# Kernel tuning notes

Hardware: AMD Instinct MI355X
Metric: run time of the kernel (lower is better)

## Reference

```python
import jax, jax.numpy as jnp
import numpy as np

B, N, E, A, H, F, HEADS = 2, 16384, 262144, 3, 128, 16, 4
DH = H // HEADS
CONST = (2.0 * np.pi) ** 0.5


def setup_inputs() -> dict:
    key = jax.random.key(0)
    ks = jax.random.split(key, 16)
    s = 0.05
    return {
        "x": jax.random.normal(ks[0], (B, N, H), jnp.float32),
        "edge_index": jax.random.randint(ks[1], (2, E), 0, N),
        # per-action message MLPs (self.mlp)
        "mlp_W1": jax.random.normal(ks[2], (A, H, H), jnp.float32) * s,
        "mlp_b1": jnp.zeros((A, H), jnp.float32),
        "mlp_W2": jax.random.normal(ks[3], (A, H, H), jnp.float32) * s,
        "mlp_b2": jnp.zeros((A, H), jnp.float32),
        # transformer (MMTs) projections, 4 heads over the action axis
        "Wq": jax.random.normal(ks[4], (H, H), jnp.float32) * s,
        "bq": jnp.zeros((H,), jnp.float32),
        "Wk": jax.random.normal(ks[5], (H, H), jnp.float32) * s,
        "bk": jnp.zeros((H,), jnp.float32),
        "Wv": jax.random.normal(ks[6], (H, H), jnp.float32) * s,
        "bv": jnp.zeros((H,), jnp.float32),
        "Wo": jax.random.normal(ks[7], (H, H), jnp.float32) * s,
        "bo": jnp.zeros((H,), jnp.float32),
        # decide_mu MLPs (decide_In_sigma is never used in the original forward)
        "mu_W1": jax.random.normal(ks[8], (A, H, H), jnp.float32) * s,
        "mu_b1": jnp.zeros((A, H), jnp.float32),
        "mu_W2": jax.random.normal(ks[9], (A, H, F), jnp.float32) * s,
        "mu_b2": jnp.zeros((A, F), jnp.float32),
    }


def _forward(x, edge_index, mlp_W1, mlp_b1, mlp_W2, mlp_b2,
             Wq, bq, Wk, bk, Wv, bv, Wo, bo, mu_W1, mu_b1, mu_W2, mu_b2):
    # per-action MLP stack: (B,N,H) -> (B,N,A,H)
    h = jax.nn.relu(jnp.einsum('bnh,ahk->bnak', x, mlp_W1) + mlp_b1)
    h = jnp.einsum('bnak,akh->bnah', h, mlp_W2) + mlp_b2
    # gather along source nodes, scatter-add into destination bins
    dst, src = edge_index[0], edge_index[1]
    g = h[:, src]                                   # (B,E,A,H) ~ 800 MB
    agg = jax.ops.segment_sum(jnp.moveaxis(g, 1, 0), dst, num_segments=N)
    agg = jnp.moveaxis(agg, 0, 1)                   # (B,N,A,H)
    # multi-head self-attention over the action axis (len A) per node
    q = (jnp.einsum('bnah,hk->bnak', agg, Wq) + bq).reshape(B, N, A, HEADS, DH)
    k = (jnp.einsum('bnah,hk->bnak', agg, Wk) + bk).reshape(B, N, A, HEADS, DH)
    v = (jnp.einsum('bnah,hk->bnak', agg, Wv) + bv).reshape(B, N, A, HEADS, DH)
    scores = jnp.einsum('bnqed,bnked->bneqk', q, k) / (DH ** 0.5)
    attn = jax.nn.softmax(scores, axis=-1)
    o = jnp.einsum('bneqk,bnked->bnqed', attn, v).reshape(B, N, A, H)
    h_I = agg + jnp.einsum('bnah,hk->bnak', o, Wo) + bo  # residual
    # per-action decode to action means: (B,N,A,F)
    m = jax.nn.relu(jnp.einsum('bnah,ahk->bnak', h_I, mu_W1) + mu_b1)
    mu = jnp.einsum('bnak,akf->bnaf', m, mu_W2) + mu_b2
    # Gaussian reparameterized sampling, VAR is a non-trainable all-ones buffer
    VAR = jnp.ones((N, A, F), jnp.float32)
    noise = jax.random.normal(jax.random.key(42), mu.shape, mu.dtype)
    sample = mu + noise * VAR
    logp = -jnp.log(CONST * VAR) - (sample - mu) ** 2 / (2.0 * VAR ** 2)
    a0 = jax.nn.softmax(jnp.tanh(sample[:, :, 0, :]), axis=-1)
    a1 = jax.nn.sigmoid(sample[:, :, 1, :])
    a2 = jnp.tanh(sample[:, :, 2, :])
    sample_out = jnp.stack([a0, a1, a2], axis=2)    # (B,N,A,F)
    return sample_out, logp.sum((-1, -2))           # ((B,N,A,F),(B,N))


def reference(x, edge_index, mlp_W1, mlp_b1, mlp_W2, mlp_b2,
              Wq, bq, Wk, bk, Wv, bv, Wo, bo, mu_W1, mu_b1, mu_W2, mu_b2):
    return _forward(x, edge_index, mlp_W1, mlp_b1, mlp_W2, mlp_b2,
                    Wq, bq, Wk, bk, Wv, bv, Wo, bo, mu_W1, mu_b1, mu_W2, mu_b2)
```

## Files before the change

kernel.cpp:

```cpp
#include <hip/hip_runtime.h>

#define NN    16384
#define EE    262144
#define BNODES 32768
#define AH    384
#define TOT_NOISE 1572864u

typedef __attribute__((ext_vector_type(8))) short short8;
typedef __attribute__((ext_vector_type(4))) float v4f;

__device__ __forceinline__ unsigned short f2bf(float f) {
  unsigned u = __float_as_uint(f);
  unsigned r = u + 0x7fffu + ((u >> 16) & 1u);
  return (unsigned short)(r >> 16);
}
__device__ __forceinline__ float bf2f(unsigned short h) {
  return __uint_as_float(((unsigned)h) << 16);
}
__device__ __forceinline__ float bflo(unsigned u) { return __uint_as_float(u << 16); }
__device__ __forceinline__ float bfhi(unsigned u) { return __uint_as_float(u & 0xffff0000u); }

__device__ __forceinline__ void threefry2x32_042(unsigned& x0, unsigned& x1) {
  const unsigned ks0 = 0u;
  const unsigned ks1 = 42u;
  const unsigned ks2 = 0x1BD11BDAu ^ 0u ^ 42u;
  x0 += ks0; x1 += ks1;
#define TFR(r) { x0 += x1; x1 = (x1 << (r)) | (x1 >> (32 - (r))); x1 ^= x0; }
  TFR(13) TFR(15) TFR(26) TFR(6)   x0 += ks1; x1 += ks2 + 1u;
  TFR(17) TFR(29) TFR(16) TFR(24)  x0 += ks2; x1 += ks0 + 2u;
  TFR(13) TFR(15) TFR(26) TFR(6)   x0 += ks0; x1 += ks1 + 3u;
  TFR(17) TFR(29) TFR(16) TFR(24)  x0 += ks1; x1 += ks2 + 4u;
  TFR(13) TFR(15) TFR(26) TFR(6)   x0 += ks2; x1 += ks0 + 5u;
#undef TFR
}

__device__ __forceinline__ float erfinv_f32(float x) {
  float w = -log1pf(-x * x);
  float p;
  if (w < 5.0f) {
    w -= 2.5f;
    p = 2.81022636e-08f;
    p = fmaf(p, w, 3.43273939e-07f);
    p = fmaf(p, w, -3.5233877e-06f);
    p = fmaf(p, w, -4.39150654e-06f);
    p = fmaf(p, w, 0.00021858087f);
    p = fmaf(p, w, -0.00125372503f);
    p = fmaf(p, w, -0.00417768164f);
    p = fmaf(p, w, 0.246640727f);
    p = fmaf(p, w, 1.50140941f);
  } else {
    w = sqrtf(w) - 3.0f;
    p = -0.000200214257f;
    p = fmaf(p, w, 0.000100950558f);
    p = fmaf(p, w, 0.00134934322f);
    p = fmaf(p, w, -0.00367342844f);
    p = fmaf(p, w, 0.00573950773f);
    p = fmaf(p, w, -0.0076224613f);
    p = fmaf(p, w, 0.00943887047f);
    p = fmaf(p, w, 1.00167406f);
    p = fmaf(p, w, 2.83297682f);
  }
  return p * x;
}

__device__ __forceinline__ unsigned jax_random_bits32(unsigned i) {
  unsigned x0 = 0u, x1 = i;
  threefry2x32_042(x0, x1);
  return x0 ^ x1;
}

__device__ __forceinline__ float jax_normal_from_bits(unsigned bits) {
  float f = __uint_as_float((bits >> 9) | 0x3f800000u) - 1.0f;
  const float lo = -0.99999994f;
  float u = f * 2.0f + lo;
  u = fmaxf(u, lo);
  return 1.4142135623730951f * erfinv_f32(u);
}

__global__ void edge_count(const int* __restrict__ dst, int* __restrict__ deg) {
  int e = blockIdx.x * 256 + threadIdx.x;
  if (e < EE) atomicAdd(&deg[dst[e]], 1);
}

__global__ __launch_bounds__(256) void scan_k(const int* __restrict__ deg,
                                              int* __restrict__ offs,
                                              int* __restrict__ cur) {
  __shared__ int part[256];
  int t = threadIdx.x;
  int base = t * 64;
  int s = 0;
  for (int i = 0; i < 64; i++) s += deg[base + i];
  part[t] = s;
  __syncthreads();
  for (int off = 1; off < 256; off <<= 1) {
    int v = (t >= off) ? part[t - off] : 0;
    __syncthreads();
    part[t] += v;
    __syncthreads();
  }
  int run = (t == 0) ? 0 : part[t - 1];
  for (int i = 0; i < 64; i++) {
    offs[base + i] = run;
    cur[base + i] = run;
    run += deg[base + i];
  }
  if (t == 255) offs[NN] = run;
}

__global__ void edge_fill(const int* __restrict__ dst, const int* __restrict__ srcv,
                          int* __restrict__ cur, int* __restrict__ csr) {
  int e = blockIdx.x * 256 + threadIdx.x;
  if (e < EE) {
    int d = dst[e];
    int p = atomicAdd(&cur[d], 1);
    csr[p] = srcv[e];
  }
}

__global__ __launch_bounds__(256) void prep_wfrag(
    const float* __restrict__ W1, const float* __restrict__ W2,
    const float* __restrict__ mW1,
    const float* __restrict__ Wq, const float* __restrict__ Wk,
    const float* __restrict__ Wv, const float* __restrict__ Wo,
    unsigned short* __restrict__ F) {
  int m = blockIdx.y;
  const float* W;
  if (m < 3) W = W1 + (long)m * 16384;
  else if (m < 6) W = W2 + (long)(m - 3) * 16384;
  else if (m < 9) W = mW1 + (long)(m - 6) * 16384;
  else W = (m == 9) ? Wq : (m == 10) ? Wk : (m == 11) ? Wv : Wo;
  int f = blockIdx.x * 256 + threadIdx.x;
  int tile = f >> 9;
  int kt = tile >> 3, nt = tile & 7;
  int r = f & 511;
  int lane = r >> 3, j = r & 7;
  int k = kt * 32 + (lane >> 4) * 8 + j;
  int n = nt * 16 + (lane & 15);
  F[(long)m * 16384 + f] = f2bf(W[k * 128 + n]);
}

__global__ __launch_bounds__(256) void prep_w2frag(
    const float* __restrict__ mW2, unsigned short* __restrict__ F2) {
  int a = blockIdx.y;
  int f = blockIdx.x * 256 + threadIdx.x;
  int kt = f >> 9;
  int r = f & 511;
  int lane = r >> 3, j = r & 7;
  int k = kt * 32 + (lane >> 4) * 8 + j;
  int n = lane & 15;
  F2[a * 2048 + f] = f2bf(mW2[(a * 128 + k) * 16 + n]);
}

#define GXSTR 136
__global__ __launch_bounds__(256, 4) void mlp_fused(
    const float* __restrict__ X,
    const unsigned short* __restrict__ WF1, const float* __restrict__ b1,
    const unsigned short* __restrict__ WF2, const float* __restrict__ b2,
    unsigned short* __restrict__ H) {
  __shared__ __align__(16) unsigned short As[128 * GXSTR];
  const int a = blockIdx.y;
  const long m0 = (long)blockIdx.x * 128;
  const int tid = threadIdx.x;
  const unsigned short* Wp1 = WF1 + (long)a * 16384;
  const unsigned short* Wp2 = WF2 + (long)a * 16384;

#pragma unroll
  for (int p = 0; p < 8; p++) {
    int c = tid + p * 256;
    int row = c >> 4, c8 = (c & 15) * 8;
    float4 v1 = *(const float4*)(X + (m0 + row) * 128 + c8);
    float4 v2 = *(const float4*)(X + (m0 + row) * 128 + c8 + 4);
    short8 o;
    o[0] = (short)f2bf(v1.x); o[1] = (short)f2bf(v1.y);
    o[2] = (short)f2bf(v1.z); o[3] = (short)f2bf(v1.w);
    o[4] = (short)f2bf(v2.x); o[5] = (short)f2bf(v2.y);
    o[6] = (short)f2bf(v2.z); o[7] = (short)f2bf(v2.w);
    *(short8*)(&As[row * GXSTR + c8]) = o;
  }
  __syncthreads();

  const int w = tid >> 6, l = tid & 63, lr = l & 15, lg = l >> 4;

  v4f acc[8][2];
#pragma unroll
  for (int mt = 0; mt < 8; mt++) {
    acc[mt][0] = (v4f){0.f, 0.f, 0.f, 0.f};
    acc[mt][1] = (v4f){0.f, 0.f, 0.f, 0.f};
  }
#pragma unroll
  for (int kt = 0; kt < 4; kt++) {
    short8 bfr[2];
#pragma unroll
    for (int ntl = 0; ntl < 2; ntl++)
      bfr[ntl] = *(const short8*)(Wp1 + (long)(kt * 8 + 2 * w + ntl) * 512 + l * 8);
#pragma unroll
    for (int mt = 0; mt < 8; mt++) {
      short8 af = *(const short8*)(&As[(mt * 16 + lr) * GXSTR + kt * 32 + lg * 8]);
      acc[mt][0] = __builtin_amdgcn_mfma_f32_16x16x32_bf16(af, bfr[0], acc[mt][0], 0, 0, 0);
      acc[mt][1] = __builtin_amdgcn_mfma_f32_16x16x32_bf16(af, bfr[1], acc[mt][1], 0, 0, 0);
    }
  }
  __syncthreads();

  {
    float bv[2] = {b1[a * 128 + 32 * w + lr], b1[a * 128 + 32 * w + 16 + lr]};
#pragma unroll
    for (int mt = 0; mt < 8; mt++)
#pragma unroll
      for (int ntl = 0; ntl < 2; ntl++)
#pragma unroll
        for (int i = 0; i < 4; i++) {
          int row = mt * 16 + lg * 4 + i;
          int col = 32 * w + ntl * 16 + lr;
          As[row * GXSTR + col] = f2bf(fmaxf(acc[mt][ntl][i] + bv[ntl], 0.0f));
        }
  }
  __syncthreads();

#pragma unroll
  for (int mt = 0; mt < 8; mt++) {
    acc[mt][0] = (v4f){0.f, 0.f, 0.f, 0.f};
    acc[mt][1] = (v4f){0.f, 0.f, 0.f, 0.f};
  }
#pragma unroll
  for (int kt = 0; kt < 4; kt++) {
    short8 bfr[2];
#pragma unroll
    for (int ntl = 0; ntl < 2; ntl++)
      bfr[ntl] = *(const short8*)(Wp2 + (long)(kt * 8 + 2 * w + ntl) * 512 + l * 8);
#pragma unroll
    for (int mt = 0; mt < 8; mt++) {
      short8 af = *(const short8*)(&As[(mt * 16 + lr) * GXSTR + kt * 32 + lg * 8]);
      acc[mt][0] = __builtin_amdgcn_mfma_f32_16x16x32_bf16(af, bfr[0], acc[mt][0], 0, 0, 0);
      acc[mt][1] = __builtin_amdgcn_mfma_f32_16x16x32_bf16(af, bfr[1], acc[mt][1], 0, 0, 0);
    }
  }
  {
    float bv[2] = {b2[a * 128 + 32 * w + lr], b2[a * 128 + 32 * w + 16 + lr]};
#pragma unroll
    for (int mt = 0; mt < 8; mt++)
#pragma unroll
      for (int ntl = 0; ntl < 2; ntl++)
#pragma unroll
        for (int i = 0; i < 4; i++) {
          long row = m0 + mt * 16 + lg * 4 + i;
          int col = 32 * w + ntl * 16 + lr;
          H[row * 384 + a * 128 + col] = f2bf(acc[mt][ntl][i] + bv[ntl]);
        }
  }
}

#define XSTR 136
#define QSTR 34
__global__ __launch_bounds__(256, 3) void attn_mega(
    const unsigned short* __restrict__ H, const int* __restrict__ offs,
    const int* __restrict__ csr,
    const unsigned short* __restrict__ WF,
    const float* __restrict__ bq, const float* __restrict__ bk,
    const float* __restrict__ bv, const float* __restrict__ bo,
    const unsigned short* __restrict__ WM1, const float* __restrict__ mb1,
    const unsigned short* __restrict__ WM2, const float* __restrict__ mb2,
    float* __restrict__ out0, float* __restrict__ out1) {
  __shared__ __align__(16) unsigned short xS[48 * XSTR];
  __shared__ __align__(16) unsigned short qS[4 * 48 * QSTR];
  __shared__ __align__(16) unsigned short kS[4 * 48 * QSTR];
  __shared__ __align__(16) unsigned short vS[4 * 48 * QSTR];
  __shared__ float lpS[48];

  const int tid = threadIdx.x;
  const long node0 = (long)blockIdx.x * 16;

  {
    const int bt = (int)(node0 >> 14);
    const int nbase = (int)(node0 & (NN - 1));
    const int nd = tid >> 4;
    const int sub = tid & 15;
    const int n = nbase + nd;
    const int e0 = offs[n], e1 = offs[n + 1];
    const unsigned short* hb = H + (long)bt * NN * 384 + sub * 24;
    float acc24[24];
#pragma unroll
    for (int i = 0; i < 24; i++) acc24[i] = 0.f;

    int j = e0;
    for (; j + 2 <= e1; j += 2) {
      int s0 = csr[j], s1 = csr[j + 1];
      const unsigned short* p0 = hb + (long)s0 * 384;
      const unsigned short* p1 = hb + (long)s1 * 384;
      uint4 A0 = *(const uint4*)(p0);
      uint4 A1 = *(const uint4*)(p0 + 8);
      uint4 A2 = *(const uint4*)(p0 + 16);
      uint4 B0 = *(const uint4*)(p1);
      uint4 B1 = *(const uint4*)(p1 + 8);
      uint4 B2 = *(const uint4*)(p1 + 16);
#define ACC8(base, u)                                                   \
      { acc24[base+0] += bflo(u.x); acc24[base+1] += bfhi(u.x);         \
        acc24[base+2] += bflo(u.y); acc24[base+3] += bfhi(u.y);         \
        acc24[base+4] += bflo(u.z); acc24[base+5] += bfhi(u.z);         \
        acc24[base+6] += bflo(u.w); acc24[base+7] += bfhi(u.w); }
      ACC8(0, A0) ACC8(8, A1) ACC8(16, A2)
      ACC8(0, B0) ACC8(8, B1) ACC8(16, B2)
    }
    if (j < e1) {
      int s0 = csr[j];
      const unsigned short* p0 = hb + (long)s0 * 384;
      uint4 A0 = *(const uint4*)(p0);
      uint4 A1 = *(const uint4*)(p0 + 8);
      uint4 A2 = *(const uint4*)(p0 + 16);
      ACC8(0, A0) ACC8(8, A1) ACC8(16, A2)
#undef ACC8
    }
#pragma unroll
    for (int jj = 0; jj < 12; jj++) {
      int g = sub * 24 + 2 * jj;
      int a_ = g >> 7;
      int c = g & 127;
      unsigned pack = (unsigned)f2bf(acc24[2 * jj]) |
                      ((unsigned)f2bf(acc24[2 * jj + 1]) << 16);
      *(unsigned*)&xS[(3 * nd + a_) * XSTR + c] = pack;
    }
  }
  __syncthreads();

  const int w = tid >> 6;
  const int l = tid & 63;
  const int lr = l & 15;
  const int lg = l >> 4;
  const unsigned short* WQ = WF;
  const unsigned short* WK = WF + 16384;
  const unsigned short* WV = WF + 32768;
  const unsigned short* WO = WF + 49152;

  v4f accq[3][2], acck[3][2], accv[3][2];
#pragma unroll
  for (int mt = 0; mt < 3; mt++)
#pragma unroll
    for (int n = 0; n < 2; n++) {
      accq[mt][n] = (v4f){0.f, 0.f, 0.f, 0.f};
      acck[mt][n] = (v4f){0.f, 0.f, 0.f, 0.f};
      accv[mt][n] = (v4f){0.f, 0.f, 0.f, 0.f};
    }
#pragma unroll
  for (int kt = 0; kt < 4; kt++) {
    short8 af[3];
#pragma unroll
    for (int mt = 0; mt < 3; mt++)
      af[mt] = *(const short8*)&xS[(mt * 16 + lr) * XSTR + kt * 32 + lg * 8];
#pragma unroll
    for (int ntl = 0; ntl < 2; ntl++) {
      long tf = (long)(kt * 8 + 2 * w + ntl) * 512 + l * 8;
      short8 b0 = *(const short8*)&WQ[tf];
      short8 b1 = *(const short8*)&WK[tf];
      short8 b2 = *(const short8*)&WV[tf];
#pragma unroll
      for (int mt = 0; mt < 3; mt++) {
        accq[mt][ntl] = __builtin_amdgcn_mfma_f32_16x16x32_bf16(af[mt], b0, accq[mt][ntl], 0, 0, 0);
        acck[mt][ntl] = __builtin_amdgcn_mfma_f32_16x16x32_bf16(af[mt], b1, acck[mt][ntl], 0, 0, 0);
        accv[mt][ntl] = __builtin_amdgcn_mfma_f32_16x16x32_bf16(af[mt], b2, accv[mt][ntl], 0, 0, 0);
      }
    }
  }
  {
    const float scale = 0.17677669529663687f;
    unsigned short* qw = &qS[w * 48 * QSTR];
    unsigned short* kw = &kS[w * 48 * QSTR];
    unsigned short* vw = &vS[w * 48 * QSTR];
    float bqv[2] = {bq[32 * w + lr], bq[32 * w + 16 + lr]};
    float bkv[2] = {bk[32 * w + lr], bk[32 * w + 16 + lr]};
    float bvv[2] = {bv[32 * w + lr], bv[32 * w + 16 + lr]};
#pragma unroll
    for (int mt = 0; mt < 3; mt++)
#pragma unroll
      for (int ntl = 0; ntl < 2; ntl++)
#pragma unroll
        for (int i = 0; i < 4; i++) {
          int row = mt * 16 + lg * 4 + i;
          int col = ntl * 16 + lr;
          qw[row * QSTR + col] = f2bf((accq[mt][ntl][i] + bqv[ntl]) * scale);
          kw[row * QSTR + col] = f2bf(acck[mt][ntl][i] + bkv[ntl]);
          vw[row * QSTR + col] = f2bf(accv[mt][ntl][i] + bvv[ntl]);
        }
  }

  float resv[3][2][4];
#pragma unroll
  for (int mt = 0; mt < 3; mt++)
#pragma unroll
    for (int ntl = 0; ntl < 2; ntl++)
#pragma unroll
      for (int i = 0; i < 4; i++)
        resv[mt][ntl][i] =
            bf2f(xS[(mt * 16 + lg * 4 + i) * XSTR + 32 * w + ntl * 16 + lr]);
  __syncthreads();

  if (l < 48) {
    int aq = l % 3;
    int ndr = l - aq;
    const unsigned* qr = (const unsigned*)&qS[(w * 48 + l) * QSTR];
    const unsigned* kr0 = (const unsigned*)&kS[(w * 48 + ndr) * QSTR];
    const unsigned* kr1 = (const unsigned*)&kS[(w * 48 + ndr + 1) * QSTR];
    const unsigned* kr2 = (const unsigned*)&kS[(w * 48 + ndr + 2) * QSTR];
    float s0 = 0.f, s1 = 0.f, s2 = 0.f;
#pragma unroll
    for (int j = 0; j < 16; j++) {
      unsigned uq = qr[j], u0 = kr0[j], u1 = kr1[j], u2 = kr2[j];
      float qa = bflo(uq), qb = bfhi(uq);
      s0 = fmaf(qa, bflo(u0), fmaf(qb, bfhi(u0), s0));
      s1 = fmaf(qa, bflo(u1), fmaf(qb, bfhi(u1), s1));
      s2 = fmaf(qa, bflo(u2), fmaf(qb, bfhi(u2), s2));
    }
    float mx = fmaxf(s0, fmaxf(s1, s2));
    float e0 = expf(s0 - mx), e1 = expf(s1 - mx), e2 = expf(s2 - mx);
    float inv = 1.0f / (e0 + e1 + e2);
    e0 *= inv; e1 *= inv; e2 *= inv;
    const unsigned* vr0 = (const unsigned*)&vS[(w * 48 + ndr) * QSTR];
    const unsigned* vr1 = (const unsigned*)&vS[(w * 48 + ndr + 1) * QSTR];
    const unsigned* vr2 = (const unsigned*)&vS[(w * 48 + ndr + 2) * QSTR];
    unsigned ov[16];
#pragma unroll
    for (int j = 0; j < 16; j++) {
      unsigned u0 = vr0[j], u1 = vr1[j], u2 = vr2[j];
      float oa = fmaf(e0, bflo(u0), fmaf(e1, bflo(u1), e2 * bflo(u2)));
      float ob = fmaf(e0, bfhi(u0), fmaf(e1, bfhi(u1), e2 * bfhi(u2)));
      ov[j] = (unsigned)f2bf(oa) | ((unsigned)f2bf(ob) << 16);
    }
    uint4* orow = (uint4*)&xS[l * XSTR + 32 * w];
    orow[0] = make_uint4(ov[0], ov[1], ov[2], ov[3]);
    orow[1] = make_uint4(ov[4], ov[5], ov[6], ov[7]);
    orow[2] = make_uint4(ov[8], ov[9], ov[10], ov[11]);
    orow[3] = make_uint4(ov[12], ov[13], ov[14], ov[15]);
  }
  __syncthreads();

  v4f acco[3][2];
#pragma unroll
  for (int mt = 0; mt < 3; mt++)
#pragma unroll
    for (int n = 0; n < 2; n++) acco[mt][n] = (v4f){0.f, 0.f, 0.f, 0.f};
#pragma unroll
  for (int kt = 0; kt < 4; kt++) {
    short8 af[3];
#pragma unroll
    for (int mt = 0; mt < 3; mt++)
      af[mt] = *(const short8*)&xS[(mt * 16 + lr) * XSTR + kt * 32 + lg * 8];
#pragma unroll
    for (int ntl = 0; ntl < 2; ntl++) {
      long tf = (long)(kt * 8 + 2 * w + ntl) * 512 + l * 8;
      short8 b = *(const short8*)&WO[tf];
#pragma unroll
      for (int mt = 0; mt < 3; mt++)
        acco[mt][ntl] = __builtin_amdgcn_mfma_f32_16x16x32_bf16(af[mt], b, acco[mt][ntl], 0, 0, 0);
    }
  }
  __syncthreads();

  {
    float bov[2] = {bo[32 * w + lr], bo[32 * w + 16 + lr]};
#pragma unroll
    for (int mt = 0; mt < 3; mt++)
#pragma unroll
      for (int ntl = 0; ntl < 2; ntl++)
#pragma unroll
        for (int i = 0; i < 4; i++) {
          int row = mt * 16 + lg * 4 + i;
          int nd = row / 3, a_ = row - nd * 3;
          int gcol = 32 * w + ntl * 16 + lr;
          xS[(a_ * 16 + nd) * XSTR + gcol] =
              f2bf(acco[mt][ntl][i] + bov[ntl] + resv[mt][ntl][i]);
        }
  }
  __syncthreads();

  v4f accm[3][2];
#pragma unroll
  for (int mt = 0; mt < 3; mt++)
#pragma unroll
    for (int n = 0; n < 2; n++) accm[mt][n] = (v4f){0.f, 0.f, 0.f, 0.f};
#pragma unroll
  for (int kt = 0; kt < 4; kt++) {
#pragma unroll
    for (int mt = 0; mt < 3; mt++) {
      short8 af = *(const short8*)&xS[(mt * 16 + lr) * XSTR + kt * 32 + lg * 8];
#pragma unroll
      for (int ntl = 0; ntl < 2; ntl++) {
        short8 b = *(const short8*)(WM1 + (long)mt * 16384 +
                                    (long)(kt * 8 + 2 * w + ntl) * 512 + l * 8);
        accm[mt][ntl] = __builtin_amdgcn_mfma_f32_16x16x32_bf16(af, b, accm[mt][ntl], 0, 0, 0);
      }
    }
  }
  __syncthreads();

#pragma unroll
  for (int mt = 0; mt < 3; mt++)
#pragma unroll
    for (int ntl = 0; ntl < 2; ntl++) {
      int col = 32 * w + ntl * 16 + lr;
      float bias = mb1[mt * 128 + col];
#pragma unroll
      for (int i = 0; i < 4; i++) {
        int rowp = mt * 16 + lg * 4 + i;
        xS[rowp * XSTR + col] = f2bf(fmaxf(accm[mt][ntl][i] + bias, 0.0f));
      }
    }
  __syncthreads();

  if (w < 3) {
    v4f accu = (v4f){0.f, 0.f, 0.f, 0.f};
#pragma unroll
    for (int kt = 0; kt < 4; kt++) {
      short8 af = *(const short8*)&xS[(w * 16 + lr) * XSTR + kt * 32 + lg * 8];
      short8 b = *(const short8*)(WM2 + w * 2048 + kt * 512 + l * 8);
      accu = __builtin_amdgcn_mfma_f32_16x16x32_bf16(af, b, accu, 0, 0, 0);
    }
    float bias = mb2[w * 16 + lr];
#pragma unroll
    for (int i = 0; i < 4; i++) {
      int nd = lg * 4 + i;
      float mu = accu[i] + bias;
      unsigned gidx = (unsigned)((node0 + nd) * 48 + w * 16 + lr);
      unsigned bits = jax_random_bits32(gidx);
      float noise = jax_normal_from_bits(bits);
      float sample = mu + noise;
      float lp = -0.9189385332046727f - 0.5f * noise * noise;
      lp += __shfl_xor(lp, 1, 64);
      lp += __shfl_xor(lp, 2, 64);
      lp += __shfl_xor(lp, 4, 64);
      lp += __shfl_xor(lp, 8, 64);
      if (lr == 0) lpS[w * 16 + nd] = lp;
      float res;
      if (w == 0) {
        float th = tanhf(sample);
        float mx = th;
        mx = fmaxf(mx, __shfl_xor(mx, 1, 64));
        mx = fmaxf(mx, __shfl_xor(mx, 2, 64));
        mx = fmaxf(mx, __shfl_xor(mx, 4, 64));
        mx = fmaxf(mx, __shfl_xor(mx, 8, 64));
        float ex = expf(th - mx);
        float ss = ex;
        ss += __shfl_xor(ss, 1, 64);
        ss += __shfl_xor(ss, 2, 64);
        ss += __shfl_xor(ss, 4, 64);
        ss += __shfl_xor(ss, 8, 64);
        res = ex / ss;
      } else if (w == 1) {
        res = 1.0f / (1.0f + expf(-sample));
      } else {
        res = tanhf(sample);
      }
      out0[gidx] = res;
    }
  }
  __syncthreads();
  if (tid < 16)
    out1[node0 + tid] = lpS[tid] + lpS[16 + tid] + lpS[32 + tid];
}

extern "C" void kernel_launch(void* const* d_in, const int* in_sizes, int n_in,
                              void* d_out, int out_size, void* d_ws, size_t ws_size,
                              hipStream_t stream) {
  const float* x = (const float*)d_in[0];
  const int* ei = (const int*)d_in[1];
  const float* W1 = (const float*)d_in[2];
  const float* b1 = (const float*)d_in[3];
  const float* W2 = (const float*)d_in[4];
  const float* b2 = (const float*)d_in[5];
  const float* Wq = (const float*)d_in[6];
  const float* bq = (const float*)d_in[7];
  const float* Wk = (const float*)d_in[8];
  const float* bk = (const float*)d_in[9];
  const float* Wv = (const float*)d_in[10];
  const float* bv = (const float*)d_in[11];
  const float* Wo = (const float*)d_in[12];
  const float* bo = (const float*)d_in[13];
  const float* mW1 = (const float*)d_in[14];
  const float* mb1 = (const float*)d_in[15];
  const float* mW2 = (const float*)d_in[16];
  const float* mb2 = (const float*)d_in[17];
  (void)in_sizes; (void)n_in; (void)out_size; (void)ws_size;

  unsigned short* HB = (unsigned short*)d_ws;
  int* deg = (int*)(HB + 12582912);
  int* offs = deg + NN;
  int* cur = offs + (NN + 1);
  int* csr = cur + NN;
  unsigned short* wfrag = (unsigned short*)(((uintptr_t)(csr + EE) + 15) & ~(uintptr_t)15);
  unsigned short* w2frag = wfrag + 13 * 16384;

  const int* dst = ei;
  const int* srcv = ei + EE;

  float* out0 = (float*)d_out;
  float* out1 = out0 + TOT_NOISE;

  hipMemsetAsync(deg, 0, NN * sizeof(int), stream);
  edge_count<<<EE / 256, 256, 0, stream>>>(dst, deg);
  scan_k<<<1, 256, 0, stream>>>(deg, offs, cur);
  edge_fill<<<EE / 256, 256, 0, stream>>>(dst, srcv, cur, csr);
  prep_wfrag<<<dim3(64, 13), 256, 0, stream>>>(W1, W2, mW1, Wq, Wk, Wv, Wo, wfrag);
  prep_w2frag<<<dim3(8, 3), 256, 0, stream>>>(mW2, w2frag);

  mlp_fused<<<dim3(BNODES / 128, 3), 256, 0, stream>>>(x, wfrag, b1, wfrag + 3 * 16384, b2, HB);
  attn_mega<<<BNODES / 16, 256, 0, stream>>>(HB, offs, csr,
                                             wfrag + 9 * 16384, bq, bk, bv, bo,
                                             wfrag + 6 * 16384, mb1, w2frag, mb2,
                                             out0, out1);
}
```

Measured before the change: 244.7 us.

## Rework scan, merge weight prep, reuse xS for Q, unroll gather, raise occupancy

The single-block scan is replaced with a 1024-thread wave-shuffle scan, and the mW2 fragment prep is folded into prep_wfrag, saving one kernel launch. In attn_mega the separate qS buffer is dropped and Q is written into xS after the residual values are moved into registers; together with a launch bound of 4 blocks per SM, this cuts LDS use to allow more resident blocks. The edge gather loop is unrolled from 2 to 4 edges to keep more loads in flight, and float-to-bf16 conversion now uses the packed intrinsic. The higher occupancy target may force register spills, and the extra barrier adds some synchronisation cost.

```diff
diff --git a/kernel.cpp b/kernel.cpp
--- a/kernel.cpp
+++ b/kernel.cpp
@@ -1,4 +1,5 @@
 #include <hip/hip_runtime.h>
+#include <hip/hip_bf16.h>
 
 #define NN    16384
 #define EE    262144
@@ -19,6 +20,10 @@
 }
 __device__ __forceinline__ float bflo(unsigned u) { return __uint_as_float(u << 16); }
 __device__ __forceinline__ float bfhi(unsigned u) { return __uint_as_float(u & 0xffff0000u); }
+__device__ __forceinline__ unsigned pk_bf16(float a, float b) {
+  __hip_bfloat162 h = __float22bfloat162_rn(make_float2(a, b));
+  return *(unsigned*)&h;
+}
 
 __device__ __forceinline__ void threefry2x32_042(unsigned& x0, unsigned& x1) {
   const unsigned ks0 = 0u;
@@ -82,29 +87,39 @@
   if (e < EE) atomicAdd(&deg[dst[e]], 1);
 }
 
-__global__ __launch_bounds__(256) void scan_k(const int* __restrict__ deg,
-                                              int* __restrict__ offs,
-                                              int* __restrict__ cur) {
-  __shared__ int part[256];
-  int t = threadIdx.x;
-  int base = t * 64;
+__global__ __launch_bounds__(1024) void scan_k(const int* __restrict__ deg,
+                                               int* __restrict__ offs,
+                                               int* __restrict__ cur) {
+  __shared__ int wsum[16];
+  const int t = threadIdx.x;
+  const int base = t * 16;
+  int loc[16];
   int s = 0;
-  for (int i = 0; i < 64; i++) s += deg[base + i];
-  part[t] = s;
-  __syncthreads();
-  for (int off = 1; off < 256; off <<= 1) {
-    int v = (t >= off) ? part[t - off] : 0;
-    __syncthreads();
-    part[t] += v;
-    __syncthreads();
-  }
-  int run = (t == 0) ? 0 : part[t - 1];
-  for (int i = 0; i < 64; i++) {
+#pragma unroll
+  for (int i = 0; i < 16; i++) { loc[i] = deg[base + i]; s += loc[i]; }
+  const int mysum = s;
+  const int lane = t & 63, wid = t >> 6;
+#pragma unroll
+  for (int off = 1; off < 64; off <<= 1) {
+    int v = __shfl_up(s, off, 64);
+    if (lane >= off) s += v;
+  }
+  if (lane == 63) wsum[wid] = s;
+  __syncthreads();
+  if (t == 0) {
+    int r = 0;
+#pragma unroll
+    for (int i = 0; i < 16; i++) { int v = wsum[i]; wsum[i] = r; r += v; }
+  }
+  __syncthreads();
+  int run = wsum[wid] + s - mysum;
+#pragma unroll
+  for (int i = 0; i < 16; i++) {
     offs[base + i] = run;
     cur[base + i] = run;
-    run += deg[base + i];
-  }
-  if (t == 255) offs[NN] = run;
+    run += loc[i];
+  }
+  if (t == 1023) offs[NN] = run;
 }
 
 __global__ void edge_fill(const int* __restrict__ dst, const int* __restrict__ srcv,
@@ -122,14 +137,28 @@
     const float* __restrict__ mW1,
     const float* __restrict__ Wq, const float* __restrict__ Wk,
     const float* __restrict__ Wv, const float* __restrict__ Wo,
+    const float* __restrict__ mW2,
     unsigned short* __restrict__ F) {
   int m = blockIdx.y;
+  int f = blockIdx.x * 256 + threadIdx.x;
+  if (m == 13) {
+    if (f < 6144) {
+      int a = f >> 11;
+      int r2 = f & 2047;
+      int kt = r2 >> 9;
+      int r = r2 & 511;
+      int lane = r >> 3, j = r & 7;
+      int k = kt * 32 + (lane >> 4) * 8 + j;
+      int n = lane & 15;
+      F[13 * 16384 + f] = f2bf(mW2[(a * 128 + k) * 16 + n]);
+    }
+    return;
+  }
   const float* W;
   if (m < 3) W = W1 + (long)m * 16384;
   else if (m < 6) W = W2 + (long)(m - 3) * 16384;
   else if (m < 9) W = mW1 + (long)(m - 6) * 16384;
   else W = (m == 9) ? Wq : (m == 10) ? Wk : (m == 11) ? Wv : Wo;
-  int f = blockIdx.x * 256 + threadIdx.x;
   int tile = f >> 9;
   int kt = tile >> 3, nt = tile & 7;
   int r = f & 511;
@@ -137,18 +166,6 @@
   int k = kt * 32 + (lane >> 4) * 8 + j;
   int n = nt * 16 + (lane & 15);
   F[(long)m * 16384 + f] = f2bf(W[k * 128 + n]);
-}
-
-__global__ __launch_bounds__(256) void prep_w2frag(
-    const float* __restrict__ mW2, unsigned short* __restrict__ F2) {
-  int a = blockIdx.y;
-  int f = blockIdx.x * 256 + threadIdx.x;
-  int kt = f >> 9;
-  int r = f & 511;
-  int lane = r >> 3, j = r & 7;
-  int k = kt * 32 + (lane >> 4) * 8 + j;
-  int n = lane & 15;
-  F2[a * 2048 + f] = f2bf(mW2[(a * 128 + k) * 16 + n]);
 }
 
 #define GXSTR 136
@@ -170,12 +187,9 @@
     int row = c >> 4, c8 = (c & 15) * 8;
     float4 v1 = *(const float4*)(X + (m0 + row) * 128 + c8);
     float4 v2 = *(const float4*)(X + (m0 + row) * 128 + c8 + 4);
-    short8 o;
-    o[0] = (short)f2bf(v1.x); o[1] = (short)f2bf(v1.y);
-    o[2] = (short)f2bf(v1.z); o[3] = (short)f2bf(v1.w);
-    o[4] = (short)f2bf(v2.x); o[5] = (short)f2bf(v2.y);
-    o[6] = (short)f2bf(v2.z); o[7] = (short)f2bf(v2.w);
-    *(short8*)(&As[row * GXSTR + c8]) = o;
+    uint4 o = make_uint4(pk_bf16(v1.x, v1.y), pk_bf16(v1.z, v1.w),
+                         pk_bf16(v2.x, v2.y), pk_bf16(v2.z, v2.w));
+    *(uint4*)(&As[row * GXSTR + c8]) = o;
   }
   __syncthreads();
 
@@ -252,7 +266,7 @@
 
 #define XSTR 136
 #define QSTR 34
-__global__ __launch_bounds__(256, 3) void attn_mega(
+__global__ __launch_bounds__(256, 4) void attn_mega(
     const unsigned short* __restrict__ H, const int* __restrict__ offs,
     const int* __restrict__ csr,
     const unsigned short* __restrict__ WF,
@@ -262,7 +276,6 @@
     const unsigned short* __restrict__ WM2, const float* __restrict__ mb2,
     float* __restrict__ out0, float* __restrict__ out1) {
   __shared__ __align__(16) unsigned short xS[48 * XSTR];
-  __shared__ __align__(16) unsigned short qS[4 * 48 * QSTR];
   __shared__ __align__(16) unsigned short kS[4 * 48 * QSTR];
   __shared__ __align__(16) unsigned short vS[4 * 48 * QSTR];
   __shared__ float lpS[48];
@@ -282,42 +295,51 @@
 #pragma unroll
     for (int i = 0; i < 24; i++) acc24[i] = 0.f;
 
+#define ACC8(base, u)                                                   \
+    { acc24[base+0] += bflo(u.x); acc24[base+1] += bfhi(u.x);           \
+      acc24[base+2] += bflo(u.y); acc24[base+3] += bfhi(u.y);           \
+      acc24[base+4] += bflo(u.z); acc24[base+5] += bfhi(u.z);           \
+      acc24[base+6] += bflo(u.w); acc24[base+7] += bfhi(u.w); }
     int j = e0;
-    for (; j + 2 <= e1; j += 2) {
-      int s0 = csr[j], s1 = csr[j + 1];
+    for (; j + 4 <= e1; j += 4) {
+      int s0 = csr[j], s1 = csr[j + 1], s2 = csr[j + 2], s3 = csr[j + 3];
       const unsigned short* p0 = hb + (long)s0 * 384;
       const unsigned short* p1 = hb + (long)s1 * 384;
+      const unsigned short* p2 = hb + (long)s2 * 384;
+      const unsigned short* p3 = hb + (long)s3 * 384;
       uint4 A0 = *(const uint4*)(p0);
       uint4 A1 = *(const uint4*)(p0 + 8);
       uint4 A2 = *(const uint4*)(p0 + 16);
       uint4 B0 = *(const uint4*)(p1);
       uint4 B1 = *(const uint4*)(p1 + 8);
       uint4 B2 = *(const uint4*)(p1 + 16);
-#define ACC8(base, u)                                                   \
-      { acc24[base+0] += bflo(u.x); acc24[base+1] += bfhi(u.x);         \
-        acc24[base+2] += bflo(u.y); acc24[base+3] += bfhi(u.y);         \
-        acc24[base+4] += bflo(u.z); acc24[base+5] += bfhi(u.z);         \
-        acc24[base+6] += bflo(u.w); acc24[base+7] += bfhi(u.w); }
+      uint4 C0 = *(const uint4*)(p2);
+      uint4 C1 = *(const uint4*)(p2 + 8);
+      uint4 C2 = *(const uint4*)(p2 + 16);
+      uint4 D0 = *(const uint4*)(p3);
+      uint4 D1 = *(const uint4*)(p3 + 8);
+      uint4 D2 = *(const uint4*)(p3 + 16);
       ACC8(0, A0) ACC8(8, A1) ACC8(16, A2)
       ACC8(0, B0) ACC8(8, B1) ACC8(16, B2)
-    }
-    if (j < e1) {
+      ACC8(0, C0) ACC8(8, C1) ACC8(16, C2)
+      ACC8(0, D0) ACC8(8, D1) ACC8(16, D2)
+    }
+    for (; j < e1; j++) {
       int s0 = csr[j];
       const unsigned short* p0 = hb + (long)s0 * 384;
       uint4 A0 = *(const uint4*)(p0);
       uint4 A1 = *(const uint4*)(p0 + 8);
       uint4 A2 = *(const uint4*)(p0 + 16);
       ACC8(0, A0) ACC8(8, A1) ACC8(16, A2)
+    }
 #undef ACC8
-    }
 #pragma unroll
     for (int jj = 0; jj < 12; jj++) {
       int g = sub * 24 + 2 * jj;
       int a_ = g >> 7;
       int c = g & 127;
-      unsigned pack = (unsigned)f2bf(acc24[2 * jj]) |
-                      ((unsigned)f2bf(acc24[2 * jj + 1]) << 16);
-      *(unsigned*)&xS[(3 * nd + a_) * XSTR + c] = pack;
+      *(unsigned*)&xS[(3 * nd + a_) * XSTR + c] =
+          pk_bf16(acc24[2 * jj], acc24[2 * jj + 1]);
     }
   }
   __syncthreads();
@@ -360,9 +382,20 @@
       }
     }
   }
+  __syncthreads();
+
+  float resv[3][2][4];
+#pragma unroll
+  for (int mt = 0; mt < 3; mt++)
+#pragma unroll
+    for (int ntl = 0; ntl < 2; ntl++)
+#pragma unroll
+      for (int i = 0; i < 4; i++)
+        resv[mt][ntl][i] =
+            bf2f(xS[(mt * 16 + lg * 4 + i) * XSTR + 32 * w + ntl * 16 + lr]);
+
   {
     const float scale = 0.17677669529663687f;
-    unsigned short* qw = &qS[w * 48 * QSTR];
     unsigned short* kw = &kS[w * 48 * QSTR];
     unsigned short* vw = &vS[w * 48 * QSTR];
     float bqv[2] = {bq[32 * w + lr], bq[32 * w + 16 + lr]};
@@ -376,27 +409,17 @@
         for (int i = 0; i < 4; i++) {
           int row = mt * 16 + lg * 4 + i;
           int col = ntl * 16 + lr;
-          qw[row * QSTR + col] = f2bf((accq[mt][ntl][i] + bqv[ntl]) * scale);
+          xS[row * XSTR + 32 * w + col] = f2bf((accq[mt][ntl][i] + bqv[ntl]) * scale);
           kw[row * QSTR + col] = f2bf(acck[mt][ntl][i] + bkv[ntl]);
           vw[row * QSTR + col] = f2bf(accv[mt][ntl][i] + bvv[ntl]);
         }
   }
-
-  float resv[3][2][4];
-#pragma unroll
-  for (int mt = 0; mt < 3; mt++)
-#pragma unroll
-    for (int ntl = 0; ntl < 2; ntl++)
-#pragma unroll
-      for (int i = 0; i < 4; i++)
-        resv[mt][ntl][i] =
-            bf2f(xS[(mt * 16 + lg * 4 + i) * XSTR + 32 * w + ntl * 16 + lr]);
   __syncthreads();
 
   if (l < 48) {
     int aq = l % 3;
     int ndr = l - aq;
-    const unsigned* qr = (const unsigned*)&qS[(w * 48 + l) * QSTR];
+    const unsigned* qr = (const unsigned*)&xS[l * XSTR + 32 * w];
     const unsigned* kr0 = (const unsigned*)&kS[(w * 48 + ndr) * QSTR];
     const unsigned* kr1 = (const unsigned*)&kS[(w * 48 + ndr + 1) * QSTR];
     const unsigned* kr2 = (const unsigned*)&kS[(w * 48 + ndr + 2) * QSTR];
@@ -422,7 +445,7 @@
       unsigned u0 = vr0[j], u1 = vr1[j], u2 = vr2[j];
       float oa = fmaf(e0, bflo(u0), fmaf(e1, bflo(u1), e2 * bflo(u2)));
       float ob = fmaf(e0, bfhi(u0), fmaf(e1, bfhi(u1), e2 * bfhi(u2)));
-      ov[j] = (unsigned)f2bf(oa) | ((unsigned)f2bf(ob) << 16);
+      ov[j] = pk_bf16(oa, ob);
     }
     uint4* orow = (uint4*)&xS[l * XSTR + 32 * w];
     orow[0] = make_uint4(ov[0], ov[1], ov[2], ov[3]);
@@ -595,10 +618,9 @@
 
   hipMemsetAsync(deg, 0, NN * sizeof(int), stream);
   edge_count<<<EE / 256, 256, 0, stream>>>(dst, deg);
-  scan_k<<<1, 256, 0, stream>>>(deg, offs, cur);
+  scan_k<<<1, 1024, 0, stream>>>(deg, offs, cur);
   edge_fill<<<EE / 256, 256, 0, stream>>>(dst, srcv, cur, csr);
-  prep_wfrag<<<dim3(64, 13), 256, 0, stream>>>(W1, W2, mW1, Wq, Wk, Wv, Wo, wfrag);
-  prep_w2frag<<<dim3(8, 3), 256, 0, stream>>>(mW2, w2frag);
+  prep_wfrag<<<dim3(64, 14), 256, 0, stream>>>(W1, W2, mW1, Wq, Wk, Wv, Wo, mW2, wfrag);
 
   mlp_fused<<<dim3(BNODES / 128, 3), 256, 0, stream>>>(x, wfrag, b1, wfrag + 3 * 16384, b2, HB);
   attn_mega<<<BNODES / 16, 256, 0, stream>>>(HB, offs, csr,
```

Measured after the change: 239.9 us. No clear change (-1.9%).
